# Optimization experiments

Hardware: AMD Instinct MI355X
Metric: run time of the kernel (lower is better)

## Reference

```python
import jax, jax.numpy as jnp
import numpy as np

B = 8192
IN = 2048
H = 2048


def setup_inputs() -> dict:
    key = jax.random.key(0)
    ks = jax.random.split(key, 16)
    s_in = 1.0 / np.sqrt(IN)
    s_h = 1.0 / np.sqrt(H)
    inp = {
        "x": jax.random.normal(ks[0], (B, IN), jnp.float32),
        "h": jax.random.normal(ks[1], (B, H), jnp.float32),
        "c": jax.random.normal(ks[2], (B, H), jnp.float32),
        # Linear weights stored torch-style as [out, in]
        "w_xf": jax.random.uniform(ks[3], (H, IN), jnp.float32, -s_in, s_in),
        "w_hf": jax.random.uniform(ks[4], (H, H), jnp.float32, -s_h, s_h),
        "b_f": jax.random.normal(ks[5], (H,), jnp.float32),
        "w_xi": jax.random.uniform(ks[6], (H, IN), jnp.float32, -s_in, s_in),
        "w_hi": jax.random.uniform(ks[7], (H, H), jnp.float32, -s_h, s_h),
        "b_i": jax.random.normal(ks[8], (H,), jnp.float32),
        "w_xo": jax.random.uniform(ks[9], (H, IN), jnp.float32, -s_in, s_in),
        "w_ho": jax.random.uniform(ks[10], (H, H), jnp.float32, -s_h, s_h),
        "b_o": jax.random.normal(ks[11], (H,), jnp.float32),
        "w_xc": jax.random.uniform(ks[12], (H, IN), jnp.float32, -s_in, s_in),
        "w_hc": jax.random.uniform(ks[13], (H, H), jnp.float32, -s_h, s_h),
        "b_c": jax.random.normal(ks[14], (H,), jnp.float32),
    }
    return inp


def reference(x, h, c, w_xf, w_hf, b_f, w_xi, w_hi, b_i,
              w_xo, w_ho, b_o, w_xc, w_hc, b_c):
    # Fuse the 8 small GEMMs into 2 batched GEMMs (x-side, h-side).
    Wx = jnp.concatenate([w_xf, w_xi, w_xo, w_xc], axis=0)  # [4H, IN]
    Wh = jnp.concatenate([w_hf, w_hi, w_ho, w_hc], axis=0)  # [4H, H]
    b = jnp.concatenate([b_f, b_i, b_o, b_c], axis=0)       # [4H]
    gates = x @ Wx.T + h @ Wh.T + b                          # [B, 4H]
    hd = h.shape[-1]
    f = jax.nn.sigmoid(gates[:, 0 * hd:1 * hd])
    i = jax.nn.sigmoid(gates[:, 1 * hd:2 * hd])
    o = jax.nn.sigmoid(gates[:, 2 * hd:3 * hd])
    c_tilde = jnp.tanh(gates[:, 3 * hd:4 * hd])
    c_new = f * c + i * c_tilde
    h_new = o * jnp.tanh(c_new)
    return (h_new, c_new)
```

## Files before the change

kernel.cpp:

```cpp
#include <hip/hip_runtime.h>


typedef __attribute__((ext_vector_type(8))) short short8;
typedef __attribute__((ext_vector_type(8))) __bf16 bf16x8;
typedef __attribute__((ext_vector_type(4))) float f32x4;

#define GLDS(gp, lp)                                                        \
  __builtin_amdgcn_global_load_lds(                                         \
      (const __attribute__((address_space(1))) void*)(gp),                  \
      (__attribute__((address_space(3))) void*)(lp), 16, 0, 0)

__device__ __forceinline__ unsigned short f2bf(float f) {
  unsigned u = __builtin_bit_cast(unsigned, f);
  u = (u + 0x7FFFu + ((u >> 16) & 1u)) >> 16;
  return (unsigned short)u;
}

__global__ void pack_x_kernel(const float* __restrict__ x,
                              const float* __restrict__ h,
                              short* __restrict__ X2) {
  long tid = (long)blockIdx.x * blockDim.x + threadIdx.x;
  long flat = tid * 8;
  int row = (int)(flat >> 12);
  int k = (int)(flat & 4095);
  const float* src = (k < 2048) ? (x + (long)row * 2048 + k)
                                : (h + (long)row * 2048 + (k - 2048));
  float4 a = *(const float4*)src;
  float4 b = *(const float4*)(src + 4);
  short8 o;
  o[0] = (short)f2bf(a.x); o[1] = (short)f2bf(a.y);
  o[2] = (short)f2bf(a.z); o[3] = (short)f2bf(a.w);
  o[4] = (short)f2bf(b.x); o[5] = (short)f2bf(b.y);
  o[6] = (short)f2bf(b.z); o[7] = (short)f2bf(b.w);
  *(short8*)(X2 + flat) = o;
}

__global__ void pack_w_kernel(const float* __restrict__ wxf, const float* __restrict__ wxi,
                              const float* __restrict__ wxo, const float* __restrict__ wxc,
                              const float* __restrict__ whf, const float* __restrict__ whi,
                              const float* __restrict__ who, const float* __restrict__ whc,
                              short* __restrict__ W3) {
  long tid = (long)blockIdx.x * blockDim.x + threadIdx.x;
  long flat = tid * 8;
  int j = (int)(flat >> 12);
  int k = (int)(flat & 4095);
  int hc = ((j >> 6) << 4) | (j & 15);
  int g = (j >> 4) & 3;
  const float* base;
  if (k < 2048) {
    const float* wx = (g == 0) ? wxf : (g == 1) ? wxi : (g == 2) ? wxo : wxc;
    base = wx + (long)hc * 2048 + k;
  } else {
    const float* wh = (g == 0) ? whf : (g == 1) ? whi : (g == 2) ? who : whc;
    base = wh + (long)hc * 2048 + (k - 2048);
  }
  float4 a = *(const float4*)base;
  float4 b = *(const float4*)(base + 4);
  short8 o;
  o[0] = (short)f2bf(a.x); o[1] = (short)f2bf(a.y);
  o[2] = (short)f2bf(a.z); o[3] = (short)f2bf(a.w);
  o[4] = (short)f2bf(b.x); o[5] = (short)f2bf(b.y);
  o[6] = (short)f2bf(b.z); o[7] = (short)f2bf(b.w);
  *(short8*)(W3 + flat) = o;
}

__global__ __launch_bounds__(512, 2) void lstm_fused_gemm(
    const short* __restrict__ X2, const short* __restrict__ W3,
    const float* __restrict__ cin,
    const float* __restrict__ bF, const float* __restrict__ bI,
    const float* __restrict__ bO, const float* __restrict__ bC,
    float* __restrict__ hout, float* __restrict__ cout_) {
  __shared__ __align__(16) short lds[65536];

  const int tid = threadIdx.x;
  const int lane = tid & 63;
  const int w = tid >> 6;
  const int wm = w >> 2;
  const int wn = w & 3;

  const int bid = blockIdx.x;
  const int bM = (bid & 7) * 4 + ((bid >> 3) & 3);
  const int bN = bid >> 5;

  const int ci = w * 64 + lane;
  const int r0 = ci >> 2;
  const int ss = (ci & 3) ^ ((r0 >> 1) & 3);
  const short* aRow0 = X2 + ((size_t)(bM * 256 + r0)) * 4096 + ss * 8;
  const short* aRow1 = aRow0 + (size_t)128 * 4096;
  const short* bRow0 = W3 + ((size_t)(bN * 256 + r0)) * 4096 + ss * 8;
  const short* bRow1 = bRow0 + (size_t)128 * 4096;
  const int wOff = w * 1024;

#define STAGE2(q, tt, bb) do {                                               \
    const int _kh = (q) >> 1;                                                \
    const short* _g0; const short* _g1;                                      \
    if ((q) == 0 || (q) == 2) {                                              \
      _g0 = aRow0 + (tt) * 64 + _kh * 32;                                    \
      _g1 = aRow1 + (tt) * 64 + _kh * 32;                                    \
    } else {                                                                 \
      _g0 = bRow0 + (tt) * 64 + _kh * 32;                                    \
      _g1 = bRow1 + (tt) * 64 + _kh * 32;                                    \
    }                                                                        \
    char* _l0 = (char*)lds + (bb) * 65536 + (q) * 16384 + wOff;              \
    GLDS(_g0, _l0);                                                          \
    GLDS(_g1, _l0 + 8192);                                                   \
  } while (0)

  const int lr = lane & 15, hi = lane >> 4;
  const int swz = ((hi ^ ((lr >> 1) & 3)) << 4);
  const int aoff = wm * 8192 + lr * 64 + swz;
  const int boff = 16384 + wn * 4096 + lr * 64 + swz;

#define LDSRD(off) (*(const bf16x8*)((const char*)lds + (off)))
#define MFMA_(a, b, c) __builtin_amdgcn_mfma_f32_16x16x32_bf16((a), (b), (c), 0, 0, 0)

  f32x4 acc[8][4] = {};

  STAGE2(0, 0, 0); STAGE2(1, 0, 0); STAGE2(3, 0, 0); STAGE2(2, 0, 0);
  asm volatile("s_waitcnt vmcnt(0)" ::: "memory");
  __builtin_amdgcn_s_barrier();

#pragma unroll 2
  for (int t = 0; t < 64; ++t) {
    const int cur = t & 1, nxt = cur ^ 1;
    const int bo = cur << 16;
    const int t1 = (t + 1) & 63;
    bf16x8 a[4], b[4];

#pragma unroll
    for (int i = 0; i < 4; ++i) a[i] = LDSRD(bo + aoff + i * 1024);
#pragma unroll
    for (int n = 0; n < 4; ++n) b[n] = LDSRD(bo + boff + n * 1024);
    STAGE2(0, t1, nxt);
    STAGE2(1, t1, nxt);
    STAGE2(3, t1, nxt);
    __builtin_amdgcn_s_barrier();
    asm volatile("s_waitcnt lgkmcnt(0)" ::: "memory");
    __builtin_amdgcn_s_setprio(1);
#pragma unroll
    for (int n = 0; n < 4; ++n)
#pragma unroll
      for (int i = 0; i < 4; ++i) acc[i][n] = MFMA_(a[i], b[n], acc[i][n]);
    __builtin_amdgcn_s_setprio(0);

#pragma unroll
    for (int i = 0; i < 4; ++i) a[i] = LDSRD(bo + aoff + (4 + i) * 1024);
    STAGE2(2, t1, nxt);
    __builtin_amdgcn_s_barrier();
    asm volatile("s_waitcnt lgkmcnt(0)" ::: "memory");
    __builtin_amdgcn_s_setprio(1);
#pragma unroll
    for (int n = 0; n < 4; ++n)
#pragma unroll
      for (int i = 0; i < 4; ++i) acc[4 + i][n] = MFMA_(a[i], b[n], acc[4 + i][n]);
    __builtin_amdgcn_s_setprio(0);
    asm volatile("s_waitcnt vmcnt(8)" ::: "memory");

#pragma unroll
    for (int i = 0; i < 4; ++i) a[i] = LDSRD(bo + aoff + 32768 + i * 1024);
#pragma unroll
    for (int n = 0; n < 4; ++n) b[n] = LDSRD(bo + boff + 32768 + n * 1024);
    __builtin_amdgcn_s_barrier();
    asm volatile("s_waitcnt lgkmcnt(0)" ::: "memory");
    __builtin_amdgcn_s_setprio(1);
#pragma unroll
    for (int n = 0; n < 4; ++n)
#pragma unroll
      for (int i = 0; i < 4; ++i) acc[i][n] = MFMA_(a[i], b[n], acc[i][n]);
    __builtin_amdgcn_s_setprio(0);

#pragma unroll
    for (int i = 0; i < 4; ++i) a[i] = LDSRD(bo + aoff + 32768 + (4 + i) * 1024);
    __builtin_amdgcn_s_barrier();
    asm volatile("s_waitcnt lgkmcnt(0)" ::: "memory");
    __builtin_amdgcn_s_setprio(1);
#pragma unroll
    for (int n = 0; n < 4; ++n)
#pragma unroll
      for (int i = 0; i < 4; ++i) acc[4 + i][n] = MFMA_(a[i], b[n], acc[4 + i][n]);
    __builtin_amdgcn_s_setprio(0);
    asm volatile("s_waitcnt vmcnt(4)" ::: "memory");
  }

  const int hc = bN * 64 + wn * 16 + lr;
  const float vbf = bF[hc], vbi = bI[hc], vbo = bO[hc], vbc = bC[hc];
#pragma unroll
  for (int m = 0; m < 8; ++m) {
    const int rbase = bM * 256 + wm * 128 + m * 16 + hi * 4;
#pragma unroll
    for (int v = 0; v < 4; ++v) {
      const size_t idx = (size_t)(rbase + v) * 2048 + hc;
      float gf = acc[m][0][v] + vbf;
      float gi = acc[m][1][v] + vbi;
      float go = acc[m][2][v] + vbo;
      float gc = acc[m][3][v] + vbc;
      float fg = 1.f / (1.f + __expf(-gf));
      float ig = 1.f / (1.f + __expf(-gi));
      float og = 1.f / (1.f + __expf(-go));
      float ct = 2.f / (1.f + __expf(-2.f * gc)) - 1.f;
      float cn = fg * cin[idx] + ig * ct;
      float hn = og * (2.f / (1.f + __expf(-2.f * cn)) - 1.f);
      hout[idx] = hn;
      cout_[idx] = cn;
    }
  }
}

extern "C" void kernel_launch(void* const* d_in, const int* in_sizes, int n_in,
                              void* d_out, int out_size, void* d_ws, size_t ws_size,
                              hipStream_t stream) {
  const float* x    = (const float*)d_in[0];
  const float* h    = (const float*)d_in[1];
  const float* c    = (const float*)d_in[2];
  const float* w_xf = (const float*)d_in[3];
  const float* w_hf = (const float*)d_in[4];
  const float* b_f  = (const float*)d_in[5];
  const float* w_xi = (const float*)d_in[6];
  const float* w_hi = (const float*)d_in[7];
  const float* b_i  = (const float*)d_in[8];
  const float* w_xo = (const float*)d_in[9];
  const float* w_ho = (const float*)d_in[10];
  const float* b_o  = (const float*)d_in[11];
  const float* w_xc = (const float*)d_in[12];
  const float* w_hc = (const float*)d_in[13];
  const float* b_c  = (const float*)d_in[14];

  float* hout  = (float*)d_out;
  float* cout_ = hout + (size_t)8192 * 2048;

  short* X2 = (short*)d_ws;
  short* W3 = X2 + (size_t)8192 * 4096;

  const int packBlocks = (int)(((long)8192 * 4096 / 8) / 256);
  pack_x_kernel<<<packBlocks, 256, 0, stream>>>(x, h, X2);
  pack_w_kernel<<<packBlocks, 256, 0, stream>>>(w_xf, w_xi, w_xo, w_xc,
                                                w_hf, w_hi, w_ho, w_hc, W3);

  lstm_fused_gemm<<<1024, 512, 0, stream>>>(X2, W3, c, b_f, b_i, b_o, b_c,
                                            hout, cout_);
}
```

Measured before the change: 542.4 us.

## Software-pipeline LDS fragment reads one MFMA phase ahead of compute

Restructures the main GEMM loop so LDS fragment loads for the next MFMA phase are issued before the current phase's MFMAs, using separate register sets (aP/aQ/aR/aS, bP/bQ). The first fragments of the next K tile are prefetched at the end of each iteration. Explicit lgkmcnt(0) waits are removed and the vmcnt waits and barriers are rearranged. The aim is to hide LDS read latency behind matrix instructions, at the cost of higher VGPR pressure and some risk of ordering hazards from the relaxed waits.

```diff
diff --git a/kernel.cpp b/kernel.cpp
--- a/kernel.cpp
+++ b/kernel.cpp
@@ -115,71 +115,71 @@
 #define MFMA_(a, b, c) __builtin_amdgcn_mfma_f32_16x16x32_bf16((a), (b), (c), 0, 0, 0)
 
   f32x4 acc[8][4] = {};
+  bf16x8 aP[4], aQ[4], aR[4], aS[4], bP[4], bQ[4];
 
   STAGE2(0, 0, 0); STAGE2(1, 0, 0); STAGE2(3, 0, 0); STAGE2(2, 0, 0);
   asm volatile("s_waitcnt vmcnt(0)" ::: "memory");
   __builtin_amdgcn_s_barrier();
+#pragma unroll
+  for (int i = 0; i < 4; ++i) aP[i] = LDSRD(aoff + i * 1024);
+#pragma unroll
+  for (int n = 0; n < 4; ++n) bP[n] = LDSRD(boff + n * 1024);
 
 #pragma unroll 2
   for (int t = 0; t < 64; ++t) {
     const int cur = t & 1, nxt = cur ^ 1;
-    const int bo = cur << 16;
+    const int bo = cur << 16, bon = nxt << 16;
     const int t1 = (t + 1) & 63;
-    bf16x8 a[4], b[4];
-
-#pragma unroll
-    for (int i = 0; i < 4; ++i) a[i] = LDSRD(bo + aoff + i * 1024);
-#pragma unroll
-    for (int n = 0; n < 4; ++n) b[n] = LDSRD(bo + boff + n * 1024);
+
+#pragma unroll
+    for (int i = 0; i < 4; ++i) aQ[i] = LDSRD(bo + aoff + (4 + i) * 1024);
     STAGE2(0, t1, nxt);
     STAGE2(1, t1, nxt);
     STAGE2(3, t1, nxt);
-    __builtin_amdgcn_s_barrier();
-    asm volatile("s_waitcnt lgkmcnt(0)" ::: "memory");
-    __builtin_amdgcn_s_setprio(1);
-#pragma unroll
-    for (int n = 0; n < 4; ++n)
-#pragma unroll
-      for (int i = 0; i < 4; ++i) acc[i][n] = MFMA_(a[i], b[n], acc[i][n]);
-    __builtin_amdgcn_s_setprio(0);
-
-#pragma unroll
-    for (int i = 0; i < 4; ++i) a[i] = LDSRD(bo + aoff + (4 + i) * 1024);
+    asm volatile("s_waitcnt vmcnt(6)" ::: "memory");
+    __builtin_amdgcn_s_barrier();
+    __builtin_amdgcn_s_setprio(1);
+#pragma unroll
+    for (int n = 0; n < 4; ++n)
+#pragma unroll
+      for (int i = 0; i < 4; ++i) acc[i][n] = MFMA_(aP[i], bP[n], acc[i][n]);
+    __builtin_amdgcn_s_setprio(0);
+
+#pragma unroll
+    for (int i = 0; i < 4; ++i) aR[i] = LDSRD(bo + aoff + 32768 + i * 1024);
+#pragma unroll
+    for (int n = 0; n < 4; ++n) bQ[n] = LDSRD(bo + boff + 32768 + n * 1024);
     STAGE2(2, t1, nxt);
     __builtin_amdgcn_s_barrier();
-    asm volatile("s_waitcnt lgkmcnt(0)" ::: "memory");
-    __builtin_amdgcn_s_setprio(1);
-#pragma unroll
-    for (int n = 0; n < 4; ++n)
-#pragma unroll
-      for (int i = 0; i < 4; ++i) acc[4 + i][n] = MFMA_(a[i], b[n], acc[4 + i][n]);
-    __builtin_amdgcn_s_setprio(0);
-    asm volatile("s_waitcnt vmcnt(8)" ::: "memory");
-
-#pragma unroll
-    for (int i = 0; i < 4; ++i) a[i] = LDSRD(bo + aoff + 32768 + i * 1024);
-#pragma unroll
-    for (int n = 0; n < 4; ++n) b[n] = LDSRD(bo + boff + 32768 + n * 1024);
-    __builtin_amdgcn_s_barrier();
-    asm volatile("s_waitcnt lgkmcnt(0)" ::: "memory");
-    __builtin_amdgcn_s_setprio(1);
-#pragma unroll
-    for (int n = 0; n < 4; ++n)
-#pragma unroll
-      for (int i = 0; i < 4; ++i) acc[i][n] = MFMA_(a[i], b[n], acc[i][n]);
-    __builtin_amdgcn_s_setprio(0);
-
-#pragma unroll
-    for (int i = 0; i < 4; ++i) a[i] = LDSRD(bo + aoff + 32768 + (4 + i) * 1024);
-    __builtin_amdgcn_s_barrier();
-    asm volatile("s_waitcnt lgkmcnt(0)" ::: "memory");
-    __builtin_amdgcn_s_setprio(1);
-#pragma unroll
-    for (int n = 0; n < 4; ++n)
-#pragma unroll
-      for (int i = 0; i < 4; ++i) acc[4 + i][n] = MFMA_(a[i], b[n], acc[4 + i][n]);
-    __builtin_amdgcn_s_setprio(0);
+    __builtin_amdgcn_s_setprio(1);
+#pragma unroll
+    for (int n = 0; n < 4; ++n)
+#pragma unroll
+      for (int i = 0; i < 4; ++i) acc[4 + i][n] = MFMA_(aQ[i], bP[n], acc[4 + i][n]);
+    __builtin_amdgcn_s_setprio(0);
+
+#pragma unroll
+    for (int i = 0; i < 4; ++i) aS[i] = LDSRD(bo + aoff + 32768 + (4 + i) * 1024);
+    __builtin_amdgcn_s_barrier();
+    __builtin_amdgcn_s_setprio(1);
+#pragma unroll
+    for (int n = 0; n < 4; ++n)
+#pragma unroll
+      for (int i = 0; i < 4; ++i) acc[i][n] = MFMA_(aR[i], bQ[n], acc[i][n]);
+    __builtin_amdgcn_s_setprio(0);
+
     asm volatile("s_waitcnt vmcnt(4)" ::: "memory");
+    __builtin_amdgcn_s_barrier();
+#pragma unroll
+    for (int i = 0; i < 4; ++i) aP[i] = LDSRD(bon + aoff + i * 1024);
+#pragma unroll
+    for (int n = 0; n < 4; ++n) bP[n] = LDSRD(bon + boff + n * 1024);
+    __builtin_amdgcn_s_setprio(1);
+#pragma unroll
+    for (int n = 0; n < 4; ++n)
+#pragma unroll
+      for (int i = 0; i < 4; ++i) acc[4 + i][n] = MFMA_(aS[i], bQ[n], acc[4 + i][n]);
+    __builtin_amdgcn_s_setprio(0);
   }
 
   const int hc = bN * 64 + wn * 16 + lr;
```

New measurement: 542.9 us. No clear change (+0.1%).
